# Kernel optimization log

Hardware: AMD Instinct MI355X
Metric: run time of the kernel (lower is better)

## Reference

```python
import jax, jax.numpy as jnp
import numpy as np

STEPS = 10          # points in t_grid -> STEPS-1 RK4 intervals
TRACE_STEPS = 2     # Hutchinson probes per dynamics eval
T_FINAL = 1.0
CLAMP = 100.0


def odefun(t, z, W1, b1, tw1, W2, b2):
    # time-conditioned 2-layer tanh MLP (canonical FFJORD dynamics)
    h = jnp.tanh(z @ W1 + b1 + t * tw1)
    return h @ W2 + b2


def setup_inputs() -> dict:
    key = jax.random.key(0)
    B, D, H = 2048, 512, 1024
    ks = jax.random.split(key, 4)
    s1 = 1.0 / np.sqrt(D)
    s2 = 1.0 / np.sqrt(H)
    return {
        "x": jax.random.normal(ks[0], (B, D), jnp.float32),
        "W1": jax.random.normal(ks[1], (D, H), jnp.float32) * s1,
        "b1": jnp.zeros((H,), jnp.float32),
        "tw1": jax.random.normal(ks[2], (H,), jnp.float32) * 0.1,
        "W2": jax.random.normal(ks[3], (H, D), jnp.float32) * s2,
        "b2": jnp.zeros((D,), jnp.float32),
    }


def reference(x, W1, b1, tw1, W2, b2):
    params = (W1, b1, tw1, W2, b2)
    B, D = x.shape

    def divergence_estimate(t, z, e):
        # torch detaches z before the grad call -> stop_gradient here
        z_sg = jax.lax.stop_gradient(z)
        f, vjp_fn = jax.vjp(lambda zz: odefun(t, zz, *params), z_sg)
        etf = vjp_fn(e)[0]                      # e^T J  (Hutchinson probe)
        return f, jnp.sum(etf * e, axis=-1)     # [B]

    def augmented_dynamics(t, state, key):
        z = state[:, :-1]                        # [B, D]
        div_est = jnp.zeros((B,), state.dtype)
        f_z = None
        for i in range(TRACE_STEPS):             # small fixed loop
            e = jax.random.randint(jax.random.fold_in(key, i), z.shape, 0, 2).astype(z.dtype) * 2.0 - 1.0
            f_z, div = divergence_estimate(t, z, e)
            div_est = div_est + div
        div_est = jnp.clip(div_est / TRACE_STEPS, -CLAMP, CLAMP)
        return jnp.concatenate([f_z, -div_est[:, None]], axis=-1)

    t_grid = jnp.linspace(0.0, T_FINAL, STEPS)
    state0 = jnp.concatenate([x, jnp.zeros((B, 1), x.dtype)], axis=-1)  # [B, D+1]

    def step(carry, t01):
        state, key = carry
        t0, t1 = t01[0], t01[1]
        dt = t1 - t0
        key, k1k, k2k, k3k, k4k = jax.random.split(key, 5)
        # torchdiffeq 'rk4' = Kutta's 3/8-rule variant (rk4_alt_step_func)
        k1 = augmented_dynamics(t0, state, k1k)
        k2 = augmented_dynamics(t0 + dt / 3.0, state + dt * k1 / 3.0, k2k)
        k3 = augmented_dynamics(t0 + dt * 2.0 / 3.0, state + dt * (k2 - k1 / 3.0), k3k)
        k4 = augmented_dynamics(t1, state + dt * (k1 - k2 + k3), k4k)
        state = state + (k1 + 3.0 * (k2 + k3) + k4) * dt * 0.125
        return (state, key), None

    t_pairs = jnp.stack([t_grid[:-1], t_grid[1:]], axis=-1)  # [STEPS-1, 2]
    (state, _), _ = jax.lax.scan(step, (state0, jax.random.key(1234)), t_pairs)

    rep, probsolve = state[:, :-1], state[:, -1]
    logprob = -0.5 * jnp.sum(rep * rep, axis=-1) + probsolve
    return rep, logprob
```

## Files before the change

kernel.cpp:

```cpp
#include <hip/hip_runtime.h>
#include <stdint.h>


#define B_N 2048
#define D_N 512
#define H_N 1024
#define BD (B_N * D_N)

typedef unsigned short u16;
typedef __attribute__((ext_vector_type(8))) short s16x8;
typedef __attribute__((ext_vector_type(4))) float f32x4;

typedef __attribute__((address_space(1))) const uint32_t ga_u32;
typedef __attribute__((address_space(3))) uint32_t ls_u32;

#if __has_builtin(__builtin_amdgcn_alignbit)
#define ROTL32(x, r) __builtin_amdgcn_alignbit((x), (x), 32 - (r))
#else
#define ROTL32(x, r) (((x) << (r)) | ((x) >> (32 - (r))))
#endif

__device__ __forceinline__ u16 f2bf(float f) {
  union { float f; uint32_t u; } c; c.f = f;
  uint32_t r = c.u + 0x7FFFu + ((c.u >> 16) & 1u);
  return (u16)(r >> 16);
}
__device__ __forceinline__ float fast_tanh(float v) {
  float e = __expf(2.0f * fabsf(v));
  float t = 1.0f - 2.0f / (e + 1.0f);
  return copysignf(t, v);
}

struct U2 { uint32_t x, y; };

__device__ __forceinline__ U2 tf2x32(uint32_t k0, uint32_t k1, uint32_t x0, uint32_t x1) {
  uint32_t k2 = k0 ^ k1 ^ 0x1BD11BDAu;
#define RND(r) { x0 += x1; x1 = ROTL32(x1, r); x1 ^= x0; }
  x0 += k0; x1 += k1;
  RND(13) RND(15) RND(26) RND(6)
  x0 += k1; x1 += k2 + 1u;
  RND(17) RND(29) RND(16) RND(24)
  x0 += k2; x1 += k0 + 2u;
  RND(13) RND(15) RND(26) RND(6)
  x0 += k0; x1 += k1 + 3u;
  RND(17) RND(29) RND(16) RND(24)
  x0 += k1; x1 += k2 + 4u;
  RND(13) RND(15) RND(26) RND(6)
  x0 += k2; x1 += k0 + 5u;
#undef RND
  U2 r; r.x = x0; r.y = x1; return r;
}

__global__ void k_keysched(uint32_t* __restrict__ ekeys) {
  if (threadIdx.x != 0 || blockIdx.x != 0) return;
  uint32_t kx = 0u, ky = 1234u;
  for (int s = 0; s < 9; ++s) {
    for (int st = 0; st < 4; ++st) {
      U2 kst = tf2x32(kx, ky, 0u, (uint32_t)(st + 1));
      for (int pr = 0; pr < 2; ++pr) {
        U2 fo = tf2x32(kst.x, kst.y, 0u, (uint32_t)pr);
        U2 k2 = tf2x32(fo.x, fo.y, 0u, 1u);
        ekeys[(s * 4 + st) * 4 + pr * 2 + 0] = k2.x;
        ekeys[(s * 4 + st) * 4 + pr * 2 + 1] = k2.y;
      }
    }
    U2 c = tf2x32(kx, ky, 0u, 0u);
    kx = c.x; ky = c.y;
  }
}

__global__ void k_egen(u16* __restrict__ ebf, const uint32_t* __restrict__ keys, int gs) {
  const int xcd = blockIdx.x & 7, bi = blockIdx.x >> 3;
  const int u = bi * 256 + threadIdx.x;
  const int slab = xcd * 4 + (u >> 13);
  const int r13 = u & 8191;
  const int stage = gs + (r13 >> 11);
  const int r11 = r13 & 2047;
  const int probe = r11 >> 10;
  const int unit = r11 & 1023;
  const uint32_t p0 = (uint32_t)(slab * 32768 + unit * 32);
  uint32_t k0 = keys[stage * 4 + probe * 2], k1 = keys[stage * 4 + probe * 2 + 1];
  uint4* dst = (uint4*)(ebf + (size_t)(stage & 3) * (2 * (size_t)BD) + (size_t)probe * BD + (size_t)p0);
#pragma unroll
  for (int g = 0; g < 4; ++g) {
    uint32_t pr[4];
#pragma unroll
    for (int h = 0; h < 4; ++h) {
      uint32_t c0 = p0 + g * 8 + h * 2;
      U2 r0 = tf2x32(k0, k1, 0u, c0);
      U2 r1 = tf2x32(k0, k1, 0u, c0 + 1u);
      pr[h] = (((r0.x ^ r0.y) & 1u) ? 0x3F80u : 0xBF80u) |
              (((r1.x ^ r1.y) & 1u) ? 0x3F800000u : 0xBF800000u);
    }
    uint4 v; v.x = pr[0]; v.y = pr[1]; v.z = pr[2]; v.w = pr[3];
    dst[g] = v;
  }
}

__global__ void k_init(const float* __restrict__ x, float* __restrict__ z, u16* __restrict__ zin,
                       float* __restrict__ lp, float* __restrict__ d0, float* __restrict__ d1) {
  int i = blockIdx.x * 256 + threadIdx.x;
  if (i < BD) { float v = x[i]; z[i] = v; zin[i] = f2bf(v); }
  if (i < B_N) { lp[i] = 0.f; d0[i] = 0.f; d1[i] = 0.f; }
}

__global__ void k_cvtT(const float* __restrict__ src, u16* __restrict__ dst, int R, int C) {
  int i = blockIdx.x * 256 + threadIdx.x;
  if (i >= R * C) return;
  int c = i / R, r = i - c * R;
  dst[i] = f2bf(src[(size_t)r * C + c]);
}
__global__ void k_cvt(const float* __restrict__ src, u16* __restrict__ dst, int n) {
  int i = blockIdx.x * 256 + threadIdx.x;
  if (i < n) dst[i] = f2bf(src[i]);
}

__global__ void k_sentinel(float* __restrict__ out, int n) {
  int i = blockIdx.x * 256 + threadIdx.x;
  if (i < n) out[i] = 12345.0f;
}


__global__ __launch_bounds__(256, 1)
void k_f1(const u16* __restrict__ zin, const u16* __restrict__ e0g, const u16* __restrict__ e1g,
          const u16* __restrict__ W1T, const u16* __restrict__ W2b,
          const float* __restrict__ b1v, const float* __restrict__ tw1v, float tstage,
          u16* __restrict__ hbuf, float* __restrict__ div0, float* __restrict__ div1) {
  __shared__ u16 S[3][14336];
  const int tid = threadIdx.x, wave = tid >> 6, lane = tid & 63;
  const int xcd = blockIdx.x & 7, idx = blockIdx.x >> 3;
  const int bm = xcd * 4 + (idx >> 3);
  const int bh = idx & 7;
  const int row0 = bm * 64, col0 = bh * 128;
  const int wm = wave >> 1, wn = wave & 1, r16 = lane & 15, q = lane >> 4;
  const int srow = lane >> 2;
  const int scol = (((lane & 3) ^ ((srow >> 1) & 3))) * 8;
  const int cqa = (q ^ ((r16 >> 1) & 3)) * 8;

  f32x4 az[2][4], au0[2][4], au1[2][4], av0[2][4], av1[2][4];
#pragma unroll
  for (int i = 0; i < 2; ++i)
#pragma unroll
    for (int j = 0; j < 4; ++j) {
      az[i][j] = (f32x4){0,0,0,0}; au0[i][j] = (f32x4){0,0,0,0}; au1[i][j] = (f32x4){0,0,0,0};
      av0[i][j] = (f32x4){0,0,0,0}; av1[i][j] = (f32x4){0,0,0,0};
    }

  const u16* gp[7];
#pragma unroll
  for (int li = 0; li < 7; ++li) {
    const int s = li * 4 + wave;
    const u16* base;
    int row;
    if (s < 12) {
      const int mat = s >> 2;
      base = (mat == 0) ? zin : (mat == 1) ? e0g : e1g;
      row = row0 + (s & 3) * 16 + srow;
    } else {
      const int t = s - 12;
      base = (t < 8) ? W1T : W2b;
      row = col0 + (t & 7) * 16 + srow;
    }
    gp[li] = base + (size_t)row * 512 + scol;
  }

  auto stage = [&](int kt, int slot) {
    u16* b = &S[slot][0];
#pragma unroll
    for (int li = 0; li < 7; ++li)
      __builtin_amdgcn_global_load_lds((ga_u32*)(gp[li] + kt),
                                       (ls_u32*)(b + (li * 4 + wave) * 512), 16, 0, 0);
  };

  auto compute = [&](int slot) {
    const u16* b = &S[slot][0];
    s16x8 zf[2], e0f[2], e1f[2], w1f[4], w2f[4];
#pragma unroll
    for (int i = 0; i < 2; ++i) {
      const int ao = (wm * 32 + i * 16 + r16) * 32 + cqa;
      zf[i]  = *(const s16x8*)(b + 0    + ao);
      e0f[i] = *(const s16x8*)(b + 2048 + ao);
      e1f[i] = *(const s16x8*)(b + 4096 + ao);
    }
#pragma unroll
    for (int j = 0; j < 4; ++j) {
      const int bo = (wn * 64 + j * 16 + r16) * 32 + cqa;
      w1f[j] = *(const s16x8*)(b + 6144  + bo);
      w2f[j] = *(const s16x8*)(b + 10240 + bo);
    }
#pragma unroll
    for (int i = 0; i < 2; ++i)
#pragma unroll
      for (int j = 0; j < 4; ++j) {
        az[i][j]  = __builtin_amdgcn_mfma_f32_16x16x32_bf16(zf[i],  w1f[j], az[i][j],  0, 0, 0);
        au0[i][j] = __builtin_amdgcn_mfma_f32_16x16x32_bf16(e0f[i], w1f[j], au0[i][j], 0, 0, 0);
        au1[i][j] = __builtin_amdgcn_mfma_f32_16x16x32_bf16(e1f[i], w1f[j], au1[i][j], 0, 0, 0);
        av0[i][j] = __builtin_amdgcn_mfma_f32_16x16x32_bf16(e0f[i], w2f[j], av0[i][j], 0, 0, 0);
        av1[i][j] = __builtin_amdgcn_mfma_f32_16x16x32_bf16(e1f[i], w2f[j], av1[i][j], 0, 0, 0);
      }
  };

  stage(0, 0);
  stage(32, 1);
  int cur = 0, nxt = 2;
  for (int it = 0; it < 15; ++it) {
    asm volatile("s_waitcnt vmcnt(7)" ::: "memory");
    __builtin_amdgcn_s_barrier();
    asm volatile("" ::: "memory");
    if (it + 2 < 16) stage((it + 2) * 32, nxt);
    compute(cur);
    if (++cur == 3) cur = 0;
    if (++nxt == 3) nxt = 0;
  }
  asm volatile("s_waitcnt vmcnt(0)" ::: "memory");
  __builtin_amdgcn_s_barrier();
  asm volatile("" ::: "memory");
  compute(cur);

  float d0s[2][4], d1s[2][4];
#pragma unroll
  for (int i = 0; i < 2; ++i)
#pragma unroll
    for (int r = 0; r < 4; ++r) { d0s[i][r] = 0.f; d1s[i][r] = 0.f; }

#pragma unroll
  for (int j = 0; j < 4; ++j) {
    const int gcol = col0 + wn * 64 + j * 16 + r16;
    const float colb = b1v[gcol] + tstage * tw1v[gcol];
#pragma unroll
    for (int i = 0; i < 2; ++i) {
      const int rbase = row0 + wm * 32 + i * 16 + q * 4;
#pragma unroll
      for (int r = 0; r < 4; ++r) {
        float hv = fast_tanh(az[i][j][r] + colb);
        hbuf[(size_t)(rbase + r) * H_N + gcol] = f2bf(hv);
        float s = 1.f - hv * hv;
        d0s[i][r] += s * au0[i][j][r] * av0[i][j][r];
        d1s[i][r] += s * au1[i][j][r] * av1[i][j][r];
      }
    }
  }
#pragma unroll
  for (int i = 0; i < 2; ++i)
#pragma unroll
    for (int r = 0; r < 4; ++r) {
      float a = d0s[i][r], bb = d1s[i][r];
#pragma unroll
      for (int m = 1; m < 16; m <<= 1) { a += __shfl_xor(a, m); bb += __shfl_xor(bb, m); }
      if (r16 == 0) {
        int grow = row0 + wm * 32 + i * 16 + q * 4 + r;
        atomicAdd(&div0[grow], a);
        atomicAdd(&div1[grow], bb);
      }
    }
}

template<int ST>
__global__ __launch_bounds__(256)
void k_f3(const u16* __restrict__ hbuf, const u16* __restrict__ W2T, const float* __restrict__ b2v,
          float* __restrict__ z, float* __restrict__ ACC, float* __restrict__ T,
          u16* __restrict__ zin, float dt,
          float* __restrict__ lp, float* __restrict__ div0, float* __restrict__ div1, float wdt) {
  __shared__ u16 S[2][3 * 2048];
  const int tid = threadIdx.x, wave = tid >> 6, lane = tid & 63;
  const int xcd = blockIdx.x & 7, idx = blockIdx.x >> 3;
  const int bm = xcd * 4 + (idx >> 4);
  const int bn = idx & 15;
  const int row0 = bm * 64, col0 = bn * 32;
  const int r16 = lane & 15, q = lane >> 4;
  const int srow = lane >> 2;
  const int scol = (((lane & 3) ^ ((srow >> 1) & 3))) * 8;
  const int cqa = (q ^ ((r16 >> 1) & 3)) * 8;

  if (bn == 0 && tid < 64) {
    int b = row0 + tid;
    float c = 0.5f * (div0[b] + div1[b]);
    c = fminf(fmaxf(c, -100.f), 100.f);
    lp[b] -= wdt * c;
    div0[b] = 0.f; div1[b] = 0.f;
  }

  f32x4 acc[2];
  acc[0] = (f32x4){0,0,0,0}; acc[1] = (f32x4){0,0,0,0};

  const size_t arow = (size_t)(row0 + wave * 16 + srow) * 1024 + scol;
  const size_t brow = (size_t)(col0 + (wave & 1) * 16 + srow) * 1024 + scol;
  auto stage = [&](int kt, int buf) {
    u16* b = &S[buf][0];
    __builtin_amdgcn_global_load_lds((ga_u32*)(hbuf + arow + kt), (ls_u32*)(b + wave * 512), 16, 0, 0);
    if (wave < 2)
      __builtin_amdgcn_global_load_lds((ga_u32*)(W2T + brow + kt), (ls_u32*)(b + 4096 + wave * 512), 16, 0, 0);
  };
  stage(0, 0);
  for (int it = 0; it < 32; ++it) {
    const int buf = it & 1;
    __syncthreads();
    if (it + 1 < 32) stage((it + 1) * 32, buf ^ 1);
    const u16* b = &S[buf][0];
    s16x8 af  = *(const s16x8*)(b + (wave * 16 + r16) * 32 + cqa);
    s16x8 bf0 = *(const s16x8*)(b + 4096 + r16 * 32 + cqa);
    s16x8 bf1 = *(const s16x8*)(b + 4096 + (16 + r16) * 32 + cqa);
    acc[0] = __builtin_amdgcn_mfma_f32_16x16x32_bf16(af, bf0, acc[0], 0, 0, 0);
    acc[1] = __builtin_amdgcn_mfma_f32_16x16x32_bf16(af, bf1, acc[1], 0, 0, 0);
  }

#pragma unroll
  for (int j = 0; j < 2; ++j) {
    const int gcol = col0 + j * 16 + r16;
    const float cb = b2v[gcol];
    const int rbase = row0 + wave * 16 + q * 4;
#pragma unroll
    for (int r = 0; r < 4; ++r) {
      const size_t idx2 = (size_t)(rbase + r) * D_N + gcol;
      const float f = acc[j][r] + cb;
      if (ST == 0) {
        ACC[idx2] = dt * 0.125f * f;
        T[idx2]   = dt * f;
        zin[idx2] = f2bf(z[idx2] + dt * f * (1.f / 3.f));
      } else if (ST == 1) {
        float t_ = T[idx2];
        ACC[idx2] += 0.375f * dt * f;
        zin[idx2] = f2bf(z[idx2] + dt * f - t_ * (1.f / 3.f));
        T[idx2]   = t_ - dt * f;
      } else if (ST == 2) {
        ACC[idx2] += 0.375f * dt * f;
        zin[idx2] = f2bf(z[idx2] + T[idx2] + dt * f);
      } else {
        float zn = z[idx2] + ACC[idx2] + dt * 0.125f * f;
        z[idx2]   = zn;
        zin[idx2] = f2bf(zn);
      }
    }
  }
}

__global__ void k_out(const float* __restrict__ z, const float* __restrict__ lp,
                      float* __restrict__ out) {
  const int xcd = blockIdx.x & 7, idx = blockIdx.x >> 3;
  const int b = (xcd * 4 + (idx >> 6)) * 64 + (idx & 63);
  int t = threadIdx.x;
  const float* zr = z + (size_t)b * D_N;
  float ss = 0.f;
  for (int d = t; d < D_N; d += 256) {
    float v = zr[d];
    out[(size_t)b * D_N + d] = v;
    ss += v * v;
  }
  for (int off = 32; off > 0; off >>= 1) ss += __shfl_down(ss, off);
  __shared__ float red[4];
  if ((t & 63) == 0) red[t >> 6] = ss;
  __syncthreads();
  if (t == 0) out[(size_t)BD + b] = -0.5f * (red[0] + red[1] + red[2] + red[3]) + lp[b];
}

extern "C" void kernel_launch(void* const* d_in, const int* in_sizes, int n_in,
                              void* d_out, int out_size, void* d_ws, size_t ws_size,
                              hipStream_t stream) {
  const float* x   = (const float*)d_in[0];
  const float* W1  = (const float*)d_in[1];
  const float* b1  = (const float*)d_in[2];
  const float* tw1 = (const float*)d_in[3];
  const float* W2  = (const float*)d_in[4];
  const float* b2  = (const float*)d_in[5];
  float* outp = (float*)d_out;

  const size_t NEEDED = (size_t)45 << 20;
  if (ws_size < NEEDED) {
    k_sentinel<<<(BD + B_N + 255) / 256, 256, 0, stream>>>(outp, BD + B_N);
    return;
  }
  char* w = (char*)d_ws;
  auto carve = [&](size_t bytes) { char* p = w; w += (bytes + 255) & ~(size_t)255; return p; };
  uint32_t* keys = (uint32_t*)carve(144 * sizeof(uint32_t));
  u16* ebf   = (u16*)carve((size_t)4 * 2 * BD * 2);
  float* z   = (float*)carve((size_t)BD * 4);
  float* ACC = (float*)carve((size_t)BD * 4);
  float* T   = (float*)carve((size_t)BD * 4);
  u16* zin   = (u16*)carve((size_t)BD * 2);
  u16* hbuf  = (u16*)carve((size_t)B_N * H_N * 2);
  u16* W1T   = (u16*)carve((size_t)H_N * D_N * 2);
  u16* W2b   = (u16*)carve((size_t)H_N * D_N * 2);
  u16* W2T   = (u16*)carve((size_t)D_N * H_N * 2);
  float* lp   = (float*)carve((size_t)B_N * 4);
  float* div0 = (float*)carve((size_t)B_N * 4);
  float* div1 = (float*)carve((size_t)B_N * 4);

  k_keysched<<<1, 1, 0, stream>>>(keys);
  k_init<<<BD / 256, 256, 0, stream>>>(x, z, zin, lp, div0, div1);
  k_cvtT<<<(D_N * H_N) / 256, 256, 0, stream>>>(W1, W1T, D_N, H_N);
  k_cvt <<<(H_N * D_N) / 256, 256, 0, stream>>>(W2, W2b, H_N * D_N);
  k_cvtT<<<(H_N * D_N) / 256, 256, 0, stream>>>(W2, W2T, H_N, D_N);

  const int gF1 = (B_N / 64) * (H_N / 128);
  const int gF3 = (B_N / 64) * (D_N / 32);

  for (int s = 0; s < 9; ++s) {
    float t0 = (float)s / 9.0f;
    float t1 = (float)(s + 1) / 9.0f;
    float dt = t1 - t0;
    float tst[4] = { t0, t0 + dt / 3.0f, t0 + dt * 2.0f / 3.0f, t1 };
    float wts[4] = { 1.f, 3.f, 3.f, 1.f };
    for (int st = 0; st < 4; ++st) {
      const int sg = s * 4 + st;
      if ((sg & 3) == 0) k_egen<<<1024, 256, 0, stream>>>(ebf, keys, sg);
      const u16* e0g = ebf + (size_t)(sg & 3) * (2 * (size_t)BD);
      const u16* e1g = e0g + BD;
      k_f1<<<gF1, 256, 0, stream>>>(zin, e0g, e1g, W1T, W2b, b1, tw1, tst[st], hbuf, div0, div1);
      const float wdt = dt * 0.125f * wts[st];
      if (st == 0)      k_f3<0><<<gF3, 256, 0, stream>>>(hbuf, W2T, b2, z, ACC, T, zin, dt, lp, div0, div1, wdt);
      else if (st == 1) k_f3<1><<<gF3, 256, 0, stream>>>(hbuf, W2T, b2, z, ACC, T, zin, dt, lp, div0, div1, wdt);
      else if (st == 2) k_f3<2><<<gF3, 256, 0, stream>>>(hbuf, W2T, b2, z, ACC, T, zin, dt, lp, div0, div1, wdt);
      else              k_f3<3><<<gF3, 256, 0, stream>>>(hbuf, W2T, b2, z, ACC, T, zin, dt, lp, div0, div1, wdt);
    }
  }
  k_out<<<B_N, 256, 0, stream>>>(z, lp, outp);
}
```

Before: 1.395 ms.

## Fuse whole RK4 integration into one persistent kernel with grid barriers

Replaces the per-stage kernel launches (probe generation, first-layer GEMM, second-layer GEMM with RK update, final output) with a single persistent 256-block kernel that loops over all 36 stages. Stages are separated by a software grid barrier built on an atomic counter. The second GEMM is retiled to 64x64 output tiles with a triple-buffered pipeline so it matches the 256-block grid. The aim is to remove launch overhead and inter-kernel gaps. The risks are spin-barrier latency and the assumption that all 256 blocks are co-resident, which would deadlock if it does not hold.

Result: slower. 2.831 ms (+103.0%).

```diff
diff --git a/kernel.cpp b/kernel.cpp
--- a/kernel.cpp
+++ b/kernel.cpp
@@ -69,39 +69,13 @@
   }
 }
 
-__global__ void k_egen(u16* __restrict__ ebf, const uint32_t* __restrict__ keys, int gs) {
-  const int xcd = blockIdx.x & 7, bi = blockIdx.x >> 3;
-  const int u = bi * 256 + threadIdx.x;
-  const int slab = xcd * 4 + (u >> 13);
-  const int r13 = u & 8191;
-  const int stage = gs + (r13 >> 11);
-  const int r11 = r13 & 2047;
-  const int probe = r11 >> 10;
-  const int unit = r11 & 1023;
-  const uint32_t p0 = (uint32_t)(slab * 32768 + unit * 32);
-  uint32_t k0 = keys[stage * 4 + probe * 2], k1 = keys[stage * 4 + probe * 2 + 1];
-  uint4* dst = (uint4*)(ebf + (size_t)(stage & 3) * (2 * (size_t)BD) + (size_t)probe * BD + (size_t)p0);
-#pragma unroll
-  for (int g = 0; g < 4; ++g) {
-    uint32_t pr[4];
-#pragma unroll
-    for (int h = 0; h < 4; ++h) {
-      uint32_t c0 = p0 + g * 8 + h * 2;
-      U2 r0 = tf2x32(k0, k1, 0u, c0);
-      U2 r1 = tf2x32(k0, k1, 0u, c0 + 1u);
-      pr[h] = (((r0.x ^ r0.y) & 1u) ? 0x3F80u : 0xBF80u) |
-              (((r1.x ^ r1.y) & 1u) ? 0x3F800000u : 0xBF800000u);
-    }
-    uint4 v; v.x = pr[0]; v.y = pr[1]; v.z = pr[2]; v.w = pr[3];
-    dst[g] = v;
-  }
-}
-
 __global__ void k_init(const float* __restrict__ x, float* __restrict__ z, u16* __restrict__ zin,
-                       float* __restrict__ lp, float* __restrict__ d0, float* __restrict__ d1) {
+                       float* __restrict__ lp, float* __restrict__ d0, float* __restrict__ d1,
+                       uint32_t* __restrict__ bar) {
   int i = blockIdx.x * 256 + threadIdx.x;
   if (i < BD) { float v = x[i]; z[i] = v; zin[i] = f2bf(v); }
   if (i < B_N) { lp[i] = 0.f; d0[i] = 0.f; d1[i] = 0.f; }
+  if (i == 0) *bar = 0u;
 }
 
 __global__ void k_cvtT(const float* __restrict__ src, u16* __restrict__ dst, int R, int C) {
@@ -120,237 +94,317 @@
   if (i < n) out[i] = 12345.0f;
 }
 
+__device__ __forceinline__ void gridbar(uint32_t* bar, uint32_t tgt) {
+  __syncthreads();
+  if (threadIdx.x == 0) {
+    __threadfence();
+    __hip_atomic_fetch_add(bar, 1u, __ATOMIC_RELAXED, __HIP_MEMORY_SCOPE_AGENT);
+    while (__hip_atomic_load(bar, __ATOMIC_RELAXED, __HIP_MEMORY_SCOPE_AGENT) < tgt)
+      __builtin_amdgcn_s_sleep(2);
+    __threadfence();
+  }
+  __syncthreads();
+}
 
 __global__ __launch_bounds__(256, 1)
-void k_f1(const u16* __restrict__ zin, const u16* __restrict__ e0g, const u16* __restrict__ e1g,
-          const u16* __restrict__ W1T, const u16* __restrict__ W2b,
-          const float* __restrict__ b1v, const float* __restrict__ tw1v, float tstage,
-          u16* __restrict__ hbuf, float* __restrict__ div0, float* __restrict__ div1) {
+void k_fused(const uint32_t* __restrict__ keys, u16* __restrict__ ebf,
+             u16* __restrict__ zin,
+             const u16* __restrict__ W1T, const u16* __restrict__ W2b, const u16* __restrict__ W2T,
+             const float* __restrict__ b1v, const float* __restrict__ tw1v, const float* __restrict__ b2v,
+             float* __restrict__ z, float* __restrict__ ACC, float* __restrict__ T,
+             u16* __restrict__ hbuf,
+             float* __restrict__ lp, float* __restrict__ div0, float* __restrict__ div1,
+             uint32_t* __restrict__ bar, float* __restrict__ outp) {
   __shared__ u16 S[3][14336];
   const int tid = threadIdx.x, wave = tid >> 6, lane = tid & 63;
   const int xcd = blockIdx.x & 7, idx = blockIdx.x >> 3;
   const int bm = xcd * 4 + (idx >> 3);
   const int bh = idx & 7;
-  const int row0 = bm * 64, col0 = bh * 128;
+  const int row0 = bm * 64;
   const int wm = wave >> 1, wn = wave & 1, r16 = lane & 15, q = lane >> 4;
   const int srow = lane >> 2;
   const int scol = (((lane & 3) ^ ((srow >> 1) & 3))) * 8;
   const int cqa = (q ^ ((r16 >> 1) & 3)) * 8;
 
-  f32x4 az[2][4], au0[2][4], au1[2][4], av0[2][4], av1[2][4];
-#pragma unroll
-  for (int i = 0; i < 2; ++i)
-#pragma unroll
-    for (int j = 0; j < 4; ++j) {
-      az[i][j] = (f32x4){0,0,0,0}; au0[i][j] = (f32x4){0,0,0,0}; au1[i][j] = (f32x4){0,0,0,0};
-      av0[i][j] = (f32x4){0,0,0,0}; av1[i][j] = (f32x4){0,0,0,0};
+  uint32_t tgt = 0;
+
+  auto egen_grp = [&](int gs) {
+#pragma unroll
+    for (int rep = 0; rep < 4; ++rep) {
+      const int uu = (idx * 256 + tid) * 4 + rep;
+      const int slab = xcd * 4 + (uu >> 13);
+      const int r13 = uu & 8191;
+      const int stg = gs + (r13 >> 11);
+      const int r11 = r13 & 2047;
+      const int probe = r11 >> 10;
+      const int unit = r11 & 1023;
+      const uint32_t p0 = (uint32_t)(slab * 32768 + unit * 32);
+      uint32_t k0 = keys[stg * 4 + probe * 2], k1 = keys[stg * 4 + probe * 2 + 1];
+      uint4* dst = (uint4*)(ebf + (size_t)(stg & 3) * (2 * (size_t)BD) + (size_t)probe * BD + (size_t)p0);
+#pragma unroll
+      for (int g = 0; g < 4; ++g) {
+        uint32_t pr[4];
+#pragma unroll
+        for (int h = 0; h < 4; ++h) {
+          uint32_t c0 = p0 + g * 8 + h * 2;
+          U2 r0 = tf2x32(k0, k1, 0u, c0);
+          U2 r1 = tf2x32(k0, k1, 0u, c0 + 1u);
+          pr[h] = (((r0.x ^ r0.y) & 1u) ? 0x3F80u : 0xBF80u) |
+                  (((r1.x ^ r1.y) & 1u) ? 0x3F800000u : 0xBF800000u);
+        }
+        uint4 v; v.x = pr[0]; v.y = pr[1]; v.z = pr[2]; v.w = pr[3];
+        dst[g] = v;
+      }
     }
-
-  const u16* gp[7];
-#pragma unroll
-  for (int li = 0; li < 7; ++li) {
-    const int s = li * 4 + wave;
-    const u16* base;
-    int row;
-    if (s < 12) {
-      const int mat = s >> 2;
-      base = (mat == 0) ? zin : (mat == 1) ? e0g : e1g;
-      row = row0 + (s & 3) * 16 + srow;
-    } else {
-      const int t = s - 12;
-      base = (t < 8) ? W1T : W2b;
-      row = col0 + (t & 7) * 16 + srow;
+  };
+
+  egen_grp(0);
+  tgt += 256; gridbar(bar, tgt);
+
+  for (int st = 0; st < 36; ++st) {
+    const int s9 = st >> 2, rsub = st & 3;
+    const float t0f = (float)s9 / 9.0f;
+    const float t1f = (float)(s9 + 1) / 9.0f;
+    const float dtt = t1f - t0f;
+    const float tstage = (rsub == 0) ? t0f : (rsub == 1) ? (t0f + dtt / 3.0f)
+                       : (rsub == 2) ? (t0f + dtt * 2.0f / 3.0f) : t1f;
+    const float wdt = dtt * 0.125f * ((rsub == 1 || rsub == 2) ? 3.0f : 1.0f);
+
+    {
+      const u16* e0g = ebf + (size_t)(st & 3) * (2 * (size_t)BD);
+      const u16* e1g = e0g + BD;
+      const int col0 = bh * 128;
+
+      f32x4 az[2][4], au0[2][4], au1[2][4], av0[2][4], av1[2][4];
+#pragma unroll
+      for (int i = 0; i < 2; ++i)
+#pragma unroll
+        for (int j = 0; j < 4; ++j) {
+          az[i][j] = (f32x4){0,0,0,0}; au0[i][j] = (f32x4){0,0,0,0}; au1[i][j] = (f32x4){0,0,0,0};
+          av0[i][j] = (f32x4){0,0,0,0}; av1[i][j] = (f32x4){0,0,0,0};
+        }
+
+      const u16* gp[7];
+#pragma unroll
+      for (int li = 0; li < 7; ++li) {
+        const int s = li * 4 + wave;
+        const u16* base;
+        int row;
+        if (s < 12) {
+          const int mat = s >> 2;
+          base = (mat == 0) ? zin : (mat == 1) ? e0g : e1g;
+          row = row0 + (s & 3) * 16 + srow;
+        } else {
+          const int t = s - 12;
+          base = (t < 8) ? W1T : W2b;
+          row = col0 + (t & 7) * 16 + srow;
+        }
+        gp[li] = base + (size_t)row * 512 + scol;
+      }
+
+      auto stg1 = [&](int kt, int slot) {
+        u16* b = &S[slot][0];
+#pragma unroll
+        for (int li = 0; li < 7; ++li)
+          __builtin_amdgcn_global_load_lds((ga_u32*)(gp[li] + kt),
+                                           (ls_u32*)(b + (li * 4 + wave) * 512), 16, 0, 0);
+      };
+      auto cmp1 = [&](int slot) {
+        const u16* b = &S[slot][0];
+        s16x8 zf[2], e0f[2], e1f[2], w1f[4], w2f[4];
+#pragma unroll
+        for (int i = 0; i < 2; ++i) {
+          const int ao = (wm * 32 + i * 16 + r16) * 32 + cqa;
+          zf[i]  = *(const s16x8*)(b + 0    + ao);
+          e0f[i] = *(const s16x8*)(b + 2048 + ao);
+          e1f[i] = *(const s16x8*)(b + 4096 + ao);
+        }
+#pragma unroll
+        for (int j = 0; j < 4; ++j) {
+          const int bo = (wn * 64 + j * 16 + r16) * 32 + cqa;
+          w1f[j] = *(const s16x8*)(b + 6144  + bo);
+          w2f[j] = *(const s16x8*)(b + 10240 + bo);
+        }
+#pragma unroll
+        for (int i = 0; i < 2; ++i)
+#pragma unroll
+          for (int j = 0; j < 4; ++j) {
+            az[i][j]  = __builtin_amdgcn_mfma_f32_16x16x32_bf16(zf[i],  w1f[j], az[i][j],  0, 0, 0);
+            au0[i][j] = __builtin_amdgcn_mfma_f32_16x16x32_bf16(e0f[i], w1f[j], au0[i][j], 0, 0, 0);
+            au1[i][j] = __builtin_amdgcn_mfma_f32_16x16x32_bf16(e1f[i], w1f[j], au1[i][j], 0, 0, 0);
+            av0[i][j] = __builtin_amdgcn_mfma_f32_16x16x32_bf16(e0f[i], w2f[j], av0[i][j], 0, 0, 0);
+            av1[i][j] = __builtin_amdgcn_mfma_f32_16x16x32_bf16(e1f[i], w2f[j], av1[i][j], 0, 0, 0);
+          }
+      };
+
+      stg1(0, 0);
+      stg1(32, 1);
+      int cur = 0, nxt = 2;
+      for (int it = 0; it < 15; ++it) {
+        asm volatile("s_waitcnt vmcnt(7)" ::: "memory");
+        __builtin_amdgcn_s_barrier();
+        asm volatile("" ::: "memory");
+        if (it + 2 < 16) stg1((it + 2) * 32, nxt);
+        cmp1(cur);
+        if (++cur == 3) cur = 0;
+        if (++nxt == 3) nxt = 0;
+      }
+      asm volatile("s_waitcnt vmcnt(0)" ::: "memory");
+      __builtin_amdgcn_s_barrier();
+      asm volatile("" ::: "memory");
+      cmp1(cur);
+
+      float d0s[2][4], d1s[2][4];
+#pragma unroll
+      for (int i = 0; i < 2; ++i)
+#pragma unroll
+        for (int rr = 0; rr < 4; ++rr) { d0s[i][rr] = 0.f; d1s[i][rr] = 0.f; }
+
+#pragma unroll
+      for (int j = 0; j < 4; ++j) {
+        const int gcol = col0 + wn * 64 + j * 16 + r16;
+        const float colb = b1v[gcol] + tstage * tw1v[gcol];
+#pragma unroll
+        for (int i = 0; i < 2; ++i) {
+          const int rbase = row0 + wm * 32 + i * 16 + q * 4;
+#pragma unroll
+          for (int rr = 0; rr < 4; ++rr) {
+            float hv = fast_tanh(az[i][j][rr] + colb);
+            hbuf[(size_t)(rbase + rr) * H_N + gcol] = f2bf(hv);
+            float sd = 1.f - hv * hv;
+            d0s[i][rr] += sd * au0[i][j][rr] * av0[i][j][rr];
+            d1s[i][rr] += sd * au1[i][j][rr] * av1[i][j][rr];
+          }
+        }
+      }
+#pragma unroll
+      for (int i = 0; i < 2; ++i)
+#pragma unroll
+        for (int rr = 0; rr < 4; ++rr) {
+          float a = d0s[i][rr], bb = d1s[i][rr];
+#pragma unroll
+          for (int m = 1; m < 16; m <<= 1) { a += __shfl_xor(a, m); bb += __shfl_xor(bb, m); }
+          if (r16 == 0) {
+            int grow = row0 + wm * 32 + i * 16 + q * 4 + rr;
+            atomicAdd(&div0[grow], a);
+            atomicAdd(&div1[grow], bb);
+          }
+        }
     }
-    gp[li] = base + (size_t)row * 512 + scol;
+    tgt += 256; gridbar(bar, tgt);
+
+    {
+      const int col0 = bh * 64;
+      u16* S3 = &S[0][0];
+
+      f32x4 a3[2][2];
+      a3[0][0] = (f32x4){0,0,0,0}; a3[0][1] = (f32x4){0,0,0,0};
+      a3[1][0] = (f32x4){0,0,0,0}; a3[1][1] = (f32x4){0,0,0,0};
+
+      const u16* gp3[2];
+      gp3[0] = hbuf + (size_t)(row0 + wave * 16 + srow) * 1024 + scol;
+      gp3[1] = W2T  + (size_t)(col0 + wave * 16 + srow) * 1024 + scol;
+
+      auto stg3 = [&](int kt, int slot) {
+        u16* b = S3 + slot * 4096;
+        __builtin_amdgcn_global_load_lds((ga_u32*)(gp3[0] + kt),
+                                         (ls_u32*)(b + wave * 512), 16, 0, 0);
+        __builtin_amdgcn_global_load_lds((ga_u32*)(gp3[1] + kt),
+                                         (ls_u32*)(b + 2048 + wave * 512), 16, 0, 0);
+      };
+      auto cmp3 = [&](int slot) {
+        const u16* b = S3 + slot * 4096;
+        s16x8 af[2], bf[2];
+#pragma unroll
+        for (int i = 0; i < 2; ++i)
+          af[i] = *(const s16x8*)(b + (wm * 32 + i * 16 + r16) * 32 + cqa);
+#pragma unroll
+        for (int j = 0; j < 2; ++j)
+          bf[j] = *(const s16x8*)(b + 2048 + (wn * 32 + j * 16 + r16) * 32 + cqa);
+#pragma unroll
+        for (int i = 0; i < 2; ++i)
+#pragma unroll
+          for (int j = 0; j < 2; ++j)
+            a3[i][j] = __builtin_amdgcn_mfma_f32_16x16x32_bf16(af[i], bf[j], a3[i][j], 0, 0, 0);
+      };
+
+      stg3(0, 0);
+      stg3(32, 1);
+
+      if (bh == 0 && tid < 64) {
+        int b = row0 + tid;
+        float c = 0.5f * (div0[b] + div1[b]);
+        c = fminf(fmaxf(c, -100.f), 100.f);
+        lp[b] -= wdt * c;
+        div0[b] = 0.f; div1[b] = 0.f;
+      }
+
+      int cur = 0, nxt = 2;
+      for (int it = 0; it < 31; ++it) {
+        asm volatile("s_waitcnt vmcnt(2)" ::: "memory");
+        __builtin_amdgcn_s_barrier();
+        asm volatile("" ::: "memory");
+        if (it + 2 < 32) stg3((it + 2) * 32, nxt);
+        cmp3(cur);
+        if (++cur == 3) cur = 0;
+        if (++nxt == 3) nxt = 0;
+      }
+      asm volatile("s_waitcnt vmcnt(0)" ::: "memory");
+      __builtin_amdgcn_s_barrier();
+      asm volatile("" ::: "memory");
+      cmp3(cur);
+
+#pragma unroll
+      for (int j = 0; j < 2; ++j) {
+        const int gcol = col0 + wn * 32 + j * 16 + r16;
+        const float cb = b2v[gcol];
+#pragma unroll
+        for (int i = 0; i < 2; ++i) {
+          const int rbase = row0 + wm * 32 + i * 16 + q * 4;
+#pragma unroll
+          for (int rr = 0; rr < 4; ++rr) {
+            const size_t idx2 = (size_t)(rbase + rr) * D_N + gcol;
+            const float f = a3[i][j][rr] + cb;
+            if (rsub == 0) {
+              ACC[idx2] = dtt * 0.125f * f;
+              T[idx2]   = dtt * f;
+              zin[idx2] = f2bf(z[idx2] + dtt * f * (1.f / 3.f));
+            } else if (rsub == 1) {
+              float t_ = T[idx2];
+              ACC[idx2] += 0.375f * dtt * f;
+              zin[idx2] = f2bf(z[idx2] + dtt * f - t_ * (1.f / 3.f));
+              T[idx2]   = t_ - dtt * f;
+            } else if (rsub == 2) {
+              ACC[idx2] += 0.375f * dtt * f;
+              zin[idx2] = f2bf(z[idx2] + T[idx2] + dtt * f);
+            } else {
+              float zn = z[idx2] + ACC[idx2] + dtt * 0.125f * f;
+              z[idx2]   = zn;
+              zin[idx2] = f2bf(zn);
+            }
+          }
+        }
+      }
+
+      if ((st & 3) == 3 && st + 1 < 36) egen_grp(st + 1);
+    }
+    tgt += 256; gridbar(bar, tgt);
   }
 
-  auto stage = [&](int kt, int slot) {
-    u16* b = &S[slot][0];
-#pragma unroll
-    for (int li = 0; li < 7; ++li)
-      __builtin_amdgcn_global_load_lds((ga_u32*)(gp[li] + kt),
-                                       (ls_u32*)(b + (li * 4 + wave) * 512), 16, 0, 0);
-  };
-
-  auto compute = [&](int slot) {
-    const u16* b = &S[slot][0];
-    s16x8 zf[2], e0f[2], e1f[2], w1f[4], w2f[4];
-#pragma unroll
-    for (int i = 0; i < 2; ++i) {
-      const int ao = (wm * 32 + i * 16 + r16) * 32 + cqa;
-      zf[i]  = *(const s16x8*)(b + 0    + ao);
-      e0f[i] = *(const s16x8*)(b + 2048 + ao);
-      e1f[i] = *(const s16x8*)(b + 4096 + ao);
-    }
-#pragma unroll
-    for (int j = 0; j < 4; ++j) {
-      const int bo = (wn * 64 + j * 16 + r16) * 32 + cqa;
-      w1f[j] = *(const s16x8*)(b + 6144  + bo);
-      w2f[j] = *(const s16x8*)(b + 10240 + bo);
-    }
-#pragma unroll
-    for (int i = 0; i < 2; ++i)
-#pragma unroll
-      for (int j = 0; j < 4; ++j) {
-        az[i][j]  = __builtin_amdgcn_mfma_f32_16x16x32_bf16(zf[i],  w1f[j], az[i][j],  0, 0, 0);
-        au0[i][j] = __builtin_amdgcn_mfma_f32_16x16x32_bf16(e0f[i], w1f[j], au0[i][j], 0, 0, 0);
-        au1[i][j] = __builtin_amdgcn_mfma_f32_16x16x32_bf16(e1f[i], w1f[j], au1[i][j], 0, 0, 0);
-        av0[i][j] = __builtin_amdgcn_mfma_f32_16x16x32_bf16(e0f[i], w2f[j], av0[i][j], 0, 0, 0);
-        av1[i][j] = __builtin_amdgcn_mfma_f32_16x16x32_bf16(e1f[i], w2f[j], av1[i][j], 0, 0, 0);
-      }
-  };
-
-  stage(0, 0);
-  stage(32, 1);
-  int cur = 0, nxt = 2;
-  for (int it = 0; it < 15; ++it) {
-    asm volatile("s_waitcnt vmcnt(7)" ::: "memory");
-    __builtin_amdgcn_s_barrier();
-    asm volatile("" ::: "memory");
-    if (it + 2 < 16) stage((it + 2) * 32, nxt);
-    compute(cur);
-    if (++cur == 3) cur = 0;
-    if (++nxt == 3) nxt = 0;
+#pragma unroll
+  for (int rr = 0; rr < 2; ++rr) {
+    const int b = bm * 64 + bh * 8 + wave * 2 + rr;
+    const float* zr = z + (size_t)b * D_N + lane * 8;
+    float4 v0 = *(const float4*)zr;
+    float4 v1 = *(const float4*)(zr + 4);
+    *(float4*)(outp + (size_t)b * D_N + lane * 8)     = v0;
+    *(float4*)(outp + (size_t)b * D_N + lane * 8 + 4) = v1;
+    float ss = v0.x*v0.x + v0.y*v0.y + v0.z*v0.z + v0.w*v0.w
+             + v1.x*v1.x + v1.y*v1.y + v1.z*v1.z + v1.w*v1.w;
+#pragma unroll
+    for (int m = 1; m < 64; m <<= 1) ss += __shfl_xor(ss, m);
+    if (lane == 0) outp[(size_t)BD + b] = -0.5f * ss + lp[b];
   }
-  asm volatile("s_waitcnt vmcnt(0)" ::: "memory");
-  __builtin_amdgcn_s_barrier();
-  asm volatile("" ::: "memory");
-  compute(cur);
-
-  float d0s[2][4], d1s[2][4];
-#pragma unroll
-  for (int i = 0; i < 2; ++i)
-#pragma unroll
-    for (int r = 0; r < 4; ++r) { d0s[i][r] = 0.f; d1s[i][r] = 0.f; }
-
-#pragma unroll
-  for (int j = 0; j < 4; ++j) {
-    const int gcol = col0 + wn * 64 + j * 16 + r16;
-    const float colb = b1v[gcol] + tstage * tw1v[gcol];
-#pragma unroll
-    for (int i = 0; i < 2; ++i) {
-      const int rbase = row0 + wm * 32 + i * 16 + q * 4;
-#pragma unroll
-      for (int r = 0; r < 4; ++r) {
-        float hv = fast_tanh(az[i][j][r] + colb);
-        hbuf[(size_t)(rbase + r) * H_N + gcol] = f2bf(hv);
-        float s = 1.f - hv * hv;
-        d0s[i][r] += s * au0[i][j][r] * av0[i][j][r];
-        d1s[i][r] += s * au1[i][j][r] * av1[i][j][r];
-      }
-    }
-  }
-#pragma unroll
-  for (int i = 0; i < 2; ++i)
-#pragma unroll
-    for (int r = 0; r < 4; ++r) {
-      float a = d0s[i][r], bb = d1s[i][r];
-#pragma unroll
-      for (int m = 1; m < 16; m <<= 1) { a += __shfl_xor(a, m); bb += __shfl_xor(bb, m); }
-      if (r16 == 0) {
-        int grow = row0 + wm * 32 + i * 16 + q * 4 + r;
-        atomicAdd(&div0[grow], a);
-        atomicAdd(&div1[grow], bb);
-      }
-    }
-}
-
-template<int ST>
-__global__ __launch_bounds__(256)
-void k_f3(const u16* __restrict__ hbuf, const u16* __restrict__ W2T, const float* __restrict__ b2v,
-          float* __restrict__ z, float* __restrict__ ACC, float* __restrict__ T,
-          u16* __restrict__ zin, float dt,
-          float* __restrict__ lp, float* __restrict__ div0, float* __restrict__ div1, float wdt) {
-  __shared__ u16 S[2][3 * 2048];
-  const int tid = threadIdx.x, wave = tid >> 6, lane = tid & 63;
-  const int xcd = blockIdx.x & 7, idx = blockIdx.x >> 3;
-  const int bm = xcd * 4 + (idx >> 4);
-  const int bn = idx & 15;
-  const int row0 = bm * 64, col0 = bn * 32;
-  const int r16 = lane & 15, q = lane >> 4;
-  const int srow = lane >> 2;
-  const int scol = (((lane & 3) ^ ((srow >> 1) & 3))) * 8;
-  const int cqa = (q ^ ((r16 >> 1) & 3)) * 8;
-
-  if (bn == 0 && tid < 64) {
-    int b = row0 + tid;
-    float c = 0.5f * (div0[b] + div1[b]);
-    c = fminf(fmaxf(c, -100.f), 100.f);
-    lp[b] -= wdt * c;
-    div0[b] = 0.f; div1[b] = 0.f;
-  }
-
-  f32x4 acc[2];
-  acc[0] = (f32x4){0,0,0,0}; acc[1] = (f32x4){0,0,0,0};
-
-  const size_t arow = (size_t)(row0 + wave * 16 + srow) * 1024 + scol;
-  const size_t brow = (size_t)(col0 + (wave & 1) * 16 + srow) * 1024 + scol;
-  auto stage = [&](int kt, int buf) {
-    u16* b = &S[buf][0];
-    __builtin_amdgcn_global_load_lds((ga_u32*)(hbuf + arow + kt), (ls_u32*)(b + wave * 512), 16, 0, 0);
-    if (wave < 2)
-      __builtin_amdgcn_global_load_lds((ga_u32*)(W2T + brow + kt), (ls_u32*)(b + 4096 + wave * 512), 16, 0, 0);
-  };
-  stage(0, 0);
-  for (int it = 0; it < 32; ++it) {
-    const int buf = it & 1;
-    __syncthreads();
-    if (it + 1 < 32) stage((it + 1) * 32, buf ^ 1);
-    const u16* b = &S[buf][0];
-    s16x8 af  = *(const s16x8*)(b + (wave * 16 + r16) * 32 + cqa);
-    s16x8 bf0 = *(const s16x8*)(b + 4096 + r16 * 32 + cqa);
-    s16x8 bf1 = *(const s16x8*)(b + 4096 + (16 + r16) * 32 + cqa);
-    acc[0] = __builtin_amdgcn_mfma_f32_16x16x32_bf16(af, bf0, acc[0], 0, 0, 0);
-    acc[1] = __builtin_amdgcn_mfma_f32_16x16x32_bf16(af, bf1, acc[1], 0, 0, 0);
-  }
-
-#pragma unroll
-  for (int j = 0; j < 2; ++j) {
-    const int gcol = col0 + j * 16 + r16;
-    const float cb = b2v[gcol];
-    const int rbase = row0 + wave * 16 + q * 4;
-#pragma unroll
-    for (int r = 0; r < 4; ++r) {
-      const size_t idx2 = (size_t)(rbase + r) * D_N + gcol;
-      const float f = acc[j][r] + cb;
-      if (ST == 0) {
-        ACC[idx2] = dt * 0.125f * f;
-        T[idx2]   = dt * f;
-        zin[idx2] = f2bf(z[idx2] + dt * f * (1.f / 3.f));
-      } else if (ST == 1) {
-        float t_ = T[idx2];
-        ACC[idx2] += 0.375f * dt * f;
-        zin[idx2] = f2bf(z[idx2] + dt * f - t_ * (1.f / 3.f));
-        T[idx2]   = t_ - dt * f;
-      } else if (ST == 2) {
-        ACC[idx2] += 0.375f * dt * f;
-        zin[idx2] = f2bf(z[idx2] + T[idx2] + dt * f);
-      } else {
-        float zn = z[idx2] + ACC[idx2] + dt * 0.125f * f;
-        z[idx2]   = zn;
-        zin[idx2] = f2bf(zn);
-      }
-    }
-  }
-}
-
-__global__ void k_out(const float* __restrict__ z, const float* __restrict__ lp,
-                      float* __restrict__ out) {
-  const int xcd = blockIdx.x & 7, idx = blockIdx.x >> 3;
-  const int b = (xcd * 4 + (idx >> 6)) * 64 + (idx & 63);
-  int t = threadIdx.x;
-  const float* zr = z + (size_t)b * D_N;
-  float ss = 0.f;
-  for (int d = t; d < D_N; d += 256) {
-    float v = zr[d];
-    out[(size_t)b * D_N + d] = v;
-    ss += v * v;
-  }
-  for (int off = 32; off > 0; off >>= 1) ss += __shfl_down(ss, off);
-  __shared__ float red[4];
-  if ((t & 63) == 0) red[t >> 6] = ss;
-  __syncthreads();
-  if (t == 0) out[(size_t)BD + b] = -0.5f * (red[0] + red[1] + red[2] + red[3]) + lp[b];
 }
 
 extern "C" void kernel_launch(void* const* d_in, const int* in_sizes, int n_in,
@@ -384,34 +438,14 @@
   float* lp   = (float*)carve((size_t)B_N * 4);
   float* div0 = (float*)carve((size_t)B_N * 4);
   float* div1 = (float*)carve((size_t)B_N * 4);
+  uint32_t* bar = (uint32_t*)carve(256);
 
   k_keysched<<<1, 1, 0, stream>>>(keys);
-  k_init<<<BD / 256, 256, 0, stream>>>(x, z, zin, lp, div0, div1);
+  k_init<<<BD / 256, 256, 0, stream>>>(x, z, zin, lp, div0, div1, bar);
   k_cvtT<<<(D_N * H_N) / 256, 256, 0, stream>>>(W1, W1T, D_N, H_N);
   k_cvt <<<(H_N * D_N) / 256, 256, 0, stream>>>(W2, W2b, H_N * D_N);
   k_cvtT<<<(H_N * D_N) / 256, 256, 0, stream>>>(W2, W2T, H_N, D_N);
 
-  const int gF1 = (B_N / 64) * (H_N / 128);
-  const int gF3 = (B_N / 64) * (D_N / 32);
-
-  for (int s = 0; s < 9; ++s) {
-    float t0 = (float)s / 9.0f;
-    float t1 = (float)(s + 1) / 9.0f;
-    float dt = t1 - t0;
-    float tst[4] = { t0, t0 + dt / 3.0f, t0 + dt * 2.0f / 3.0f, t1 };
-    float wts[4] = { 1.f, 3.f, 3.f, 1.f };
-    for (int st = 0; st < 4; ++st) {
-      const int sg = s * 4 + st;
-      if ((sg & 3) == 0) k_egen<<<1024, 256, 0, stream>>>(ebf, keys, sg);
-      const u16* e0g = ebf + (size_t)(sg & 3) * (2 * (size_t)BD);
-      const u16* e1g = e0g + BD;
-      k_f1<<<gF1, 256, 0, stream>>>(zin, e0g, e1g, W1T, W2b, b1, tw1, tst[st], hbuf, div0, div1);
-      const float wdt = dt * 0.125f * wts[st];
-      if (st == 0)      k_f3<0><<<gF3, 256, 0, stream>>>(hbuf, W2T, b2, z, ACC, T, zin, dt, lp, div0, div1, wdt);
-      else if (st == 1) k_f3<1><<<gF3, 256, 0, stream>>>(hbuf, W2T, b2, z, ACC, T, zin, dt, lp, div0, div1, wdt);
-      else if (st == 2) k_f3<2><<<gF3, 256, 0, stream>>>(hbuf, W2T, b2, z, ACC, T, zin, dt, lp, div0, div1, wdt);
-      else              k_f3<3><<<gF3, 256, 0, stream>>>(hbuf, W2T, b2, z, ACC, T, zin, dt, lp, div0, div1, wdt);
-    }
-  }
-  k_out<<<B_N, 256, 0, stream>>>(z, lp, outp);
-}
+  k_fused<<<256, 256, 0, stream>>>(keys, ebf, zin, W1T, W2b, W2T, b1, tw1, b2,
+                                   z, ACC, T, hbuf, lp, div0, div1, bar, outp);
+}
```
